# Kernel tuning notes

Measured on AMD Instinct MI355X. Metric: run time of the kernel, lower is better.

Reference implementation:

```python
import jax, jax.numpy as jnp
import numpy as np

N_NODES = 50000
N_EDGES = 800000
NODE_F = 100     # memory_feats
EDGE_F = 100     # raw edge feature dim
TIME_D = 100     # temporal encoder dimension
HEADS = 2
OUT_F = 100
NEG_SLOPE = 0.2


def setup_inputs() -> dict:
    key = jax.random.key(0)
    ks = jax.random.split(key, 16)
    return {
        'memory': jax.random.normal(ks[0], (N_NODES, NODE_F), jnp.float32),
        'node_ts': jax.random.uniform(ks[1], (N_NODES,), jnp.float32),
        'edge_feats_raw': jax.random.normal(ks[2], (N_EDGES, EDGE_F), jnp.float32),
        'edge_ts': jax.random.uniform(ks[3], (N_EDGES,), jnp.float32),
        'time_w': jax.random.normal(ks[4], (TIME_D,), jnp.float32),
        'time_b': jax.random.normal(ks[5], (TIME_D,), jnp.float32),
        'fc_node_w': jax.random.normal(ks[6], (NODE_F, HEADS * OUT_F), jnp.float32) * 0.1,
        'fc_node_b': jax.random.normal(ks[7], (HEADS * OUT_F,), jnp.float32) * 0.1,
        'fc_edge_w': jax.random.normal(ks[8], (EDGE_F + TIME_D, HEADS * OUT_F), jnp.float32) * 0.1,
        'fc_edge_b': jax.random.normal(ks[9], (HEADS * OUT_F,), jnp.float32) * 0.1,
        'attn_l': jax.random.normal(ks[10], (HEADS, OUT_F), jnp.float32) * 0.1,
        'attn_r': jax.random.normal(ks[11], (HEADS, OUT_F), jnp.float32) * 0.1,
        'attn_e': jax.random.normal(ks[12], (HEADS, OUT_F), jnp.float32) * 0.1,
        'src': jax.random.randint(ks[13], (N_EDGES,), 0, N_NODES, jnp.int32),
        'dst': jax.random.randint(ks[14], (N_EDGES,), 0, N_NODES, jnp.int32),
    }


def _forward(memory, node_ts, edge_feats_raw, edge_ts,
             time_w, time_b, fc_node_w, fc_node_b, fc_edge_w, fc_edge_b,
             attn_l, attn_r, attn_e, src, dst):
    n = memory.shape[0]
    # TemporalEdgePreprocess: Fourier time encoding of (edge_ts - ts[src])
    time_diff = edge_ts - node_ts[src]                                  # [E]
    te = jnp.cos(time_diff[:, None] * time_w[None, :] + time_b[None, :])  # [E, T]
    efeat = jnp.concatenate([edge_feats_raw, te], axis=1)               # [E, EDGE_F+T]

    # EdgeGATConv (eval mode: dropouts are identity)
    node_feat = (memory @ fc_node_w + fc_node_b).reshape(n, HEADS, OUT_F)          # [N,H,F]
    edge_feat = (efeat @ fc_edge_w + fc_edge_b).reshape(-1, HEADS, OUT_F)          # [E,H,F]

    el = jnp.einsum('nhf,hf->nh', node_feat, attn_l)   # [N,H]
    er = jnp.einsum('nhf,hf->nh', node_feat, attn_r)   # [N,H]
    ee = jnp.einsum('ehf,hf->eh', edge_feat, attn_e)   # [E,H]

    el_prime = el[src] + ee                             # u_add_e  [E,H]
    e = el_prime + er[dst]                              # e_add_v  [E,H]
    e = jnp.where(e > 0, e, NEG_SLOPE * e)              # leaky_relu

    # edge_softmax: softmax over incoming edges per destination node, per head
    emax = jax.ops.segment_max(e, dst, num_segments=n)  # [N,H]
    emax = jnp.where(jnp.isfinite(emax), emax, 0.0)     # zero-in-degree safety
    e_exp = jnp.exp(e - emax[dst])                      # [E,H]
    denom = jax.ops.segment_sum(e_exp, dst, num_segments=n)  # [N,H]
    a = e_exp / denom[dst]                              # [E,H]

    # msg_fn: m = a * el_prime (el_prime has singleton feature dim in torch code)
    m = a * el_prime                                    # [E,H]
    ft = jax.ops.segment_sum(m, dst, num_segments=n)    # [N,H]  (== [N,H,1] features)

    # residual: Identity since memory_feats == out_feats -> view(N,-1,F) = [N,1,F]
    rst = ft[:, :, None] + memory[:, None, :]           # [N,H,F] via broadcast
    return rst.mean(axis=1)                             # .mean(1) over heads -> [N,F]


def reference(memory, node_ts, edge_feats_raw, edge_ts,
              time_w, time_b, fc_node_w, fc_node_b, fc_edge_w, fc_edge_b,
              attn_l, attn_r, attn_e, src, dst):
    return _forward(memory, node_ts, edge_feats_raw, edge_ts,
                    time_w, time_b, fc_node_w, fc_node_b, fc_edge_w, fc_edge_b,
                    attn_l, attn_r, attn_e, src, dst)
```

## Files before the change

kernel.cpp:

```cpp
#include <hip/hip_runtime.h>


constexpr int F = 100;
constexpr float NEG_SLOPE = 0.2f;
constexpr int EPB = 32;

__device__ __forceinline__ float wave_reduce(float v) {
#pragma unroll
    for (int off = 32; off > 0; off >>= 1)
        v += __shfl_down(v, off, 64);
    return v;
}

__global__ void precompute_kernel(
    const float* __restrict__ fc_node_w, const float* __restrict__ fc_node_b,
    const float* __restrict__ fc_edge_w, const float* __restrict__ fc_edge_b,
    const float* __restrict__ attn_l, const float* __restrict__ attn_r,
    const float* __restrict__ attn_e,
    float4* __restrict__ w_node, float2* __restrict__ w_edge,
    float* __restrict__ bias)
{
    int wid  = blockIdx.x * (blockDim.x >> 6) + (threadIdx.x >> 6);
    int lane = threadIdx.x & 63;
    if (wid < F) {
        int t = wid;
        float a0 = 0.f, a1 = 0.f, a2 = 0.f, a3 = 0.f;
        for (int f = lane; f < F; f += 64) {
            float w0 = fc_node_w[t * 2 * F + f];
            float w1 = fc_node_w[t * 2 * F + F + f];
            a0 += w0 * attn_l[f];
            a1 += w1 * attn_l[F + f];
            a2 += w0 * attn_r[f];
            a3 += w1 * attn_r[F + f];
        }
        a0 = wave_reduce(a0); a1 = wave_reduce(a1);
        a2 = wave_reduce(a2); a3 = wave_reduce(a3);
        if (lane == 0) w_node[t] = make_float4(a0, a1, a2, a3);
    } else if (wid < 3 * F) {
        int t = wid - F;
        float a0 = 0.f, a1 = 0.f;
        for (int f = lane; f < F; f += 64) {
            a0 += fc_edge_w[t * 2 * F + f] * attn_e[f];
            a1 += fc_edge_w[t * 2 * F + F + f] * attn_e[F + f];
        }
        a0 = wave_reduce(a0); a1 = wave_reduce(a1);
        if (lane == 0) w_edge[t] = make_float2(a0, a1);
    } else if (wid < 3 * F + 6) {
        int j = wid - 3 * F;
        const float* b  = (j < 4) ? fc_node_b : fc_edge_b;
        const float* av = (j < 2) ? attn_l : (j < 4 ? attn_r : attn_e);
        int h = j & 1;
        float a0 = 0.f;
        for (int f = lane; f < F; f += 64)
            a0 += b[h * F + f] * av[h * F + f];
        a0 = wave_reduce(a0);
        if (lane == 0) bias[j] = a0;
    }
}

__global__ void node_kernel(const float* __restrict__ memory,
                            const float4* __restrict__ w_node,
                            const float* __restrict__ bias,
                            float4* __restrict__ el_er,
                            int* __restrict__ cnt, int N)
{
    int n    = blockIdx.x * (blockDim.x >> 6) + (threadIdx.x >> 6);
    int lane = threadIdx.x & 63;
    if (n >= N) return;
    const float* mrow = memory + (size_t)n * F;
    float a0 = 0.f, a1 = 0.f, a2 = 0.f, a3 = 0.f;
    for (int k = lane; k < F; k += 64) {
        float m  = mrow[k];
        float4 w = w_node[k];
        a0 += m * w.x; a1 += m * w.y; a2 += m * w.z; a3 += m * w.w;
    }
    a0 = wave_reduce(a0); a1 = wave_reduce(a1);
    a2 = wave_reduce(a2); a3 = wave_reduce(a3);
    if (lane == 0)
        el_er[n] = make_float4(a0 + bias[0], a1 + bias[1],
                               a2 + bias[2], a3 + bias[3]);
    if (lane == 1)
        cnt[n] = 0;
}

__global__ void count_kernel(const int* __restrict__ dst,
                             int* __restrict__ cnt, int E)
{
    int i = blockIdx.x * blockDim.x + threadIdx.x;
    if (i < E) atomicAdd(&cnt[dst[i]], 1);
}

__global__ void scan1_kernel(const int* __restrict__ cnt,
                             int* __restrict__ offs,
                             int* __restrict__ bsum, int N)
{
    __shared__ int tmp[256];
    int i = blockIdx.x * 256 + threadIdx.x;
    int v = (i < N) ? cnt[i] : 0;
    tmp[threadIdx.x] = v;
    __syncthreads();
    for (int d = 1; d < 256; d <<= 1) {
        int t = (threadIdx.x >= d) ? tmp[threadIdx.x - d] : 0;
        __syncthreads();
        tmp[threadIdx.x] += t;
        __syncthreads();
    }
    if (i < N) offs[i] = tmp[threadIdx.x] - v;
    if (threadIdx.x == 255) bsum[blockIdx.x] = tmp[255];
}

__global__ void scan2_kernel(int* __restrict__ bsum, int nb)
{
    __shared__ int tmp[256];
    int v = (threadIdx.x < nb) ? bsum[threadIdx.x] : 0;
    tmp[threadIdx.x] = v;
    __syncthreads();
    for (int d = 1; d < 256; d <<= 1) {
        int t = (threadIdx.x >= d) ? tmp[threadIdx.x - d] : 0;
        __syncthreads();
        tmp[threadIdx.x] += t;
        __syncthreads();
    }
    if (threadIdx.x < nb) bsum[threadIdx.x] = tmp[threadIdx.x] - v;
}

__global__ void scan3_kernel(int* __restrict__ offs,
                             const int* __restrict__ bsum,
                             int* __restrict__ cursor, int N)
{
    int i = blockIdx.x * 256 + threadIdx.x;
    if (i < N) {
        int o = offs[i] + bsum[blockIdx.x];
        offs[i]   = o;
        cursor[i] = o;
    }
}

__global__ void edge_gemv_kernel(
    const float* __restrict__ edge_raw,
    const float* __restrict__ edge_ts,
    const float* __restrict__ node_ts,
    const int* __restrict__ src,
    const int* __restrict__ dst,
    const float* __restrict__ time_w,
    const float* __restrict__ time_b,
    const float2* __restrict__ w_edge,
    const float* __restrict__ bias,
    const float4* __restrict__ el_er,
    int* __restrict__ cursor,
    float4* __restrict__ bucket, int E)
{
    __shared__ float4 wx4[25], wy4[25], wz4[25], ww4[25], tw4[25], tb4[25];
    __shared__ float  td_s[EPB];
    __shared__ float2 el_s[EPB];
    __shared__ float2 er_s[EPB];
    __shared__ int    d_s[EPB];

    const int  t  = threadIdx.x;
    const long eb = (long)blockIdx.x * EPB;

    if (t < 25) {
        float4 x, y, z, w, tw, tb;
#pragma unroll
        for (int j = 0; j < 4; ++j) {
            int k = 4 * t + j;
            float2 wr = w_edge[k];
            float2 wt = w_edge[F + k];
            ((float*)&x)[j]  = wr.x;  ((float*)&y)[j]  = wr.y;
            ((float*)&z)[j]  = wt.x;  ((float*)&w)[j]  = wt.y;
            ((float*)&tw)[j] = time_w[k];
            ((float*)&tb)[j] = time_b[k];
        }
        wx4[t] = x; wy4[t] = y; wz4[t] = z; ww4[t] = w;
        tw4[t] = tw; tb4[t] = tb;
    } else if (t >= 64 && t < 64 + EPB) {
        int  l = t - 64;
        long e = eb + l;
        if (e < E) {
            int s = src[e], d = dst[e];
            d_s[l]  = d;
            td_s[l] = edge_ts[e] - node_ts[s];
            float4 a = el_er[s];
            float4 b = el_er[d];
            el_s[l] = make_float2(a.x, a.y);
            er_s[l] = make_float2(b.z, b.w);
        }
    }
    __syncthreads();

    const int  el_ = t >> 3;
    const int  s8  = t & 7;
    const long e   = eb + el_;
    float a0 = 0.f, a1 = 0.f;
    if (e < E) {
        const float  td   = td_s[el_];
        const float4* row = (const float4*)edge_raw + e * 25;
#pragma unroll
        for (int i = 0; i < 4; ++i) {
            int c = s8 + 8 * i;
            if (c < 25) {
                float4 r  = row[c];
                float4 x  = wx4[c], y = wy4[c], z = wz4[c], w = ww4[c];
                float4 tw = tw4[c], tb = tb4[c];
                float c0 = __cosf(fmaf(td, tw.x, tb.x));
                float c1 = __cosf(fmaf(td, tw.y, tb.y));
                float c2 = __cosf(fmaf(td, tw.z, tb.z));
                float c3 = __cosf(fmaf(td, tw.w, tb.w));
                a0 = fmaf(r.x, x.x, fmaf(c0, z.x, a0));
                a1 = fmaf(r.x, y.x, fmaf(c0, w.x, a1));
                a0 = fmaf(r.y, x.y, fmaf(c1, z.y, a0));
                a1 = fmaf(r.y, y.y, fmaf(c1, w.y, a1));
                a0 = fmaf(r.z, x.z, fmaf(c2, z.z, a0));
                a1 = fmaf(r.z, y.z, fmaf(c2, w.z, a1));
                a0 = fmaf(r.w, x.w, fmaf(c3, z.w, a0));
                a1 = fmaf(r.w, y.w, fmaf(c3, w.w, a1));
            }
        }
    }
    a0 += __shfl_down(a0, 4, 64);  a1 += __shfl_down(a1, 4, 64);
    a0 += __shfl_down(a0, 2, 64);  a1 += __shfl_down(a1, 2, 64);
    a0 += __shfl_down(a0, 1, 64);  a1 += __shfl_down(a1, 1, 64);

    if (s8 == 0 && e < E) {
        float elp0 = el_s[el_].x + a0 + bias[4];
        float elp1 = el_s[el_].y + a1 + bias[5];
        float e0 = elp0 + er_s[el_].x;
        float e1 = elp1 + er_s[el_].y;
        e0 = e0 > 0.f ? e0 : NEG_SLOPE * e0;
        e1 = e1 > 0.f ? e1 : NEG_SLOPE * e1;
        float x0 = __expf(e0);
        float x1 = __expf(e1);
        int pos = atomicAdd(&cursor[d_s[el_]], 1);
        bucket[pos] = make_float4(x0 * elp0, x1 * elp1, x0, x1);
    }
}

__global__ void reduce_kernel(const float4* __restrict__ bucket,
                              const int* __restrict__ offs,
                              const int* __restrict__ cnt,
                              float* __restrict__ addbuf, int N)
{
    int g = blockIdx.x * (blockDim.x >> 4) + (threadIdx.x >> 4);
    int l = threadIdx.x & 15;
    if (g >= N) return;
    int base = offs[g];
    int deg  = cnt[g];
    float s0 = 0.f, s1 = 0.f, s2 = 0.f, s3 = 0.f;
    for (int j = l; j < deg; j += 16) {
        float4 v = bucket[base + j];
        s0 += v.x; s1 += v.y; s2 += v.z; s3 += v.w;
    }
    s0 += __shfl_down(s0, 8, 64); s1 += __shfl_down(s1, 8, 64);
    s2 += __shfl_down(s2, 8, 64); s3 += __shfl_down(s3, 8, 64);
    s0 += __shfl_down(s0, 4, 64); s1 += __shfl_down(s1, 4, 64);
    s2 += __shfl_down(s2, 4, 64); s3 += __shfl_down(s3, 4, 64);
    s0 += __shfl_down(s0, 2, 64); s1 += __shfl_down(s1, 2, 64);
    s2 += __shfl_down(s2, 2, 64); s3 += __shfl_down(s3, 2, 64);
    s0 += __shfl_down(s0, 1, 64); s1 += __shfl_down(s1, 1, 64);
    s2 += __shfl_down(s2, 1, 64); s3 += __shfl_down(s3, 1, 64);
    if (l == 0) {
        float ft0 = (s2 != 0.f) ? s0 / s2 : 0.f;
        float ft1 = (s3 != 0.f) ? s1 / s3 : 0.f;
        addbuf[g] = 0.5f * (ft0 + ft1);
    }
}

__global__ void out_kernel(const float* __restrict__ memory,
                           const float* __restrict__ addbuf,
                           float* __restrict__ out, int N)
{
    int i = blockIdx.x * blockDim.x + threadIdx.x;
    int total = N * (F / 2);
    if (i >= total) return;
    int n = i / (F / 2);
    float add = addbuf[n];
    float2 m = ((const float2*)memory)[i];
    float2 o;
    o.x = m.x + add;
    o.y = m.y + add;
    ((float2*)out)[i] = o;
}

extern "C" void kernel_launch(void* const* d_in, const int* in_sizes, int n_in,
                              void* d_out, int out_size, void* d_ws, size_t ws_size,
                              hipStream_t stream)
{
    const float* memory     = (const float*)d_in[0];
    const float* node_ts    = (const float*)d_in[1];
    const float* edge_raw   = (const float*)d_in[2];
    const float* edge_ts    = (const float*)d_in[3];
    const float* time_w     = (const float*)d_in[4];
    const float* time_b     = (const float*)d_in[5];
    const float* fc_node_w  = (const float*)d_in[6];
    const float* fc_node_b  = (const float*)d_in[7];
    const float* fc_edge_w  = (const float*)d_in[8];
    const float* fc_edge_b  = (const float*)d_in[9];
    const float* attn_l     = (const float*)d_in[10];
    const float* attn_r     = (const float*)d_in[11];
    const float* attn_e     = (const float*)d_in[12];
    const int*   src        = (const int*)d_in[13];
    const int*   dst        = (const int*)d_in[14];
    float*       out        = (float*)d_out;

    const int N = in_sizes[1];
    const int E = in_sizes[3];

    float* ws = (float*)d_ws;
    float4* w_node  = (float4*)ws;
    float2* w_edge  = (float2*)(ws + 400);
    float*  bias    = ws + 800;
    float4* el_er   = (float4*)(ws + 816);
    float*  addbuf  = ws + 816 + 4 * (size_t)N;
    int*    cnt     = (int*)(ws + 816 + 5 * (size_t)N);
    int*    offs    = cnt + N;
    int*    cursor  = offs + N;
    int*    bsum    = cursor + N;
    size_t  boff    = 816 + 8 * (size_t)N + 256;
    boff            = (boff + 3) & ~(size_t)3;
    float4* bucket  = (float4*)(ws + boff);

    const int nb = (N + 255) / 256;

    {
        int waves  = 3 * F + 6;
        int blocks = (waves + 3) / 4;
        precompute_kernel<<<blocks, 256, 0, stream>>>(
            fc_node_w, fc_node_b, fc_edge_w, fc_edge_b,
            attn_l, attn_r, attn_e, w_node, w_edge, bias);
    }
    {
        int blocks = (N + 3) / 4;
        node_kernel<<<blocks, 256, 0, stream>>>(
            memory, w_node, bias, el_er, cnt, N);
    }
    {
        int blocks = (E + 255) / 256;
        count_kernel<<<blocks, 256, 0, stream>>>(dst, cnt, E);
    }
    scan1_kernel<<<nb, 256, 0, stream>>>(cnt, offs, bsum, N);
    scan2_kernel<<<1, 256, 0, stream>>>(bsum, nb);
    scan3_kernel<<<nb, 256, 0, stream>>>(offs, bsum, cursor, N);
    {
        int blocks = (E + EPB - 1) / EPB;
        edge_gemv_kernel<<<blocks, 256, 0, stream>>>(
            edge_raw, edge_ts, node_ts, src, dst, time_w, time_b,
            w_edge, bias, el_er, cursor, bucket, E);
    }
    {
        int blocks = (N + 15) / 16;
        reduce_kernel<<<blocks, 256, 0, stream>>>(bucket, offs, cnt, addbuf, N);
    }
    {
        int total  = N * (F / 2);
        int blocks = (total + 255) / 256;
        out_kernel<<<blocks, 256, 0, stream>>>(memory, addbuf, out, N);
    }
}
```

Before: 553.1 us.

## Fuse small kernels to cut launch count and intermediate traffic

```diff
diff --git a/kernel.cpp b/kernel.cpp
--- a/kernel.cpp
+++ b/kernel.cpp
@@ -18,7 +18,8 @@
     const float* __restrict__ attn_l, const float* __restrict__ attn_r,
     const float* __restrict__ attn_e,
     float4* __restrict__ w_node, float2* __restrict__ w_edge,
-    float* __restrict__ bias)
+    float* __restrict__ bias,
+    int* __restrict__ cnt, int N)
 {
     int wid  = blockIdx.x * (blockDim.x >> 6) + (threadIdx.x >> 6);
     int lane = threadIdx.x & 63;
@@ -56,38 +57,39 @@
         a0 = wave_reduce(a0);
         if (lane == 0) bias[j] = a0;
     }
-}
-
-__global__ void node_kernel(const float* __restrict__ memory,
-                            const float4* __restrict__ w_node,
-                            const float* __restrict__ bias,
-                            float4* __restrict__ el_er,
-                            int* __restrict__ cnt, int N)
-{
-    int n    = blockIdx.x * (blockDim.x >> 6) + (threadIdx.x >> 6);
-    int lane = threadIdx.x & 63;
-    if (n >= N) return;
-    const float* mrow = memory + (size_t)n * F;
-    float a0 = 0.f, a1 = 0.f, a2 = 0.f, a3 = 0.f;
-    for (int k = lane; k < F; k += 64) {
-        float m  = mrow[k];
-        float4 w = w_node[k];
-        a0 += m * w.x; a1 += m * w.y; a2 += m * w.z; a3 += m * w.w;
-    }
-    a0 = wave_reduce(a0); a1 = wave_reduce(a1);
-    a2 = wave_reduce(a2); a3 = wave_reduce(a3);
-    if (lane == 0)
-        el_er[n] = make_float4(a0 + bias[0], a1 + bias[1],
-                               a2 + bias[2], a3 + bias[3]);
-    if (lane == 1)
-        cnt[n] = 0;
-}
-
-__global__ void count_kernel(const int* __restrict__ dst,
-                             int* __restrict__ cnt, int E)
-{
-    int i = blockIdx.x * blockDim.x + threadIdx.x;
-    if (i < E) atomicAdd(&cnt[dst[i]], 1);
+    for (int i = blockIdx.x * blockDim.x + threadIdx.x; i < N;
+         i += gridDim.x * blockDim.x)
+        cnt[i] = 0;
+}
+
+__global__ void node_count_kernel(const float* __restrict__ memory,
+                                  const float4* __restrict__ w_node,
+                                  const float* __restrict__ bias,
+                                  float4* __restrict__ el_er,
+                                  const int* __restrict__ dst,
+                                  int* __restrict__ cnt,
+                                  int N, int E, int nodeBlocks)
+{
+    if ((int)blockIdx.x < nodeBlocks) {
+        int n    = blockIdx.x * (blockDim.x >> 6) + (threadIdx.x >> 6);
+        int lane = threadIdx.x & 63;
+        if (n >= N) return;
+        const float* mrow = memory + (size_t)n * F;
+        float a0 = 0.f, a1 = 0.f, a2 = 0.f, a3 = 0.f;
+        for (int k = lane; k < F; k += 64) {
+            float m  = mrow[k];
+            float4 w = w_node[k];
+            a0 += m * w.x; a1 += m * w.y; a2 += m * w.z; a3 += m * w.w;
+        }
+        a0 = wave_reduce(a0); a1 = wave_reduce(a1);
+        a2 = wave_reduce(a2); a3 = wave_reduce(a3);
+        if (lane == 0)
+            el_er[n] = make_float4(a0 + bias[0], a1 + bias[1],
+                                   a2 + bias[2], a3 + bias[3]);
+    } else {
+        int i = (blockIdx.x - nodeBlocks) * blockDim.x + threadIdx.x;
+        if (i < E) atomicAdd(&cnt[dst[i]], 1);
+    }
 }
 
 __global__ void scan1_kernel(const int* __restrict__ cnt,
@@ -109,28 +111,25 @@
     if (threadIdx.x == 255) bsum[blockIdx.x] = tmp[255];
 }
 
-__global__ void scan2_kernel(int* __restrict__ bsum, int nb)
+__global__ void scan23_kernel(int* __restrict__ offs,
+                              const int* __restrict__ bsum,
+                              int* __restrict__ cursor, int N, int nb)
 {
     __shared__ int tmp[256];
-    int v = (threadIdx.x < nb) ? bsum[threadIdx.x] : 0;
-    tmp[threadIdx.x] = v;
+    int t = threadIdx.x;
+    int v = (t < nb) ? bsum[t] : 0;
+    tmp[t] = v;
     __syncthreads();
     for (int d = 1; d < 256; d <<= 1) {
-        int t = (threadIdx.x >= d) ? tmp[threadIdx.x - d] : 0;
+        int x = (t >= d) ? tmp[t - d] : 0;
         __syncthreads();
-        tmp[threadIdx.x] += t;
+        tmp[t] += x;
         __syncthreads();
     }
-    if (threadIdx.x < nb) bsum[threadIdx.x] = tmp[threadIdx.x] - v;
-}
-
-__global__ void scan3_kernel(int* __restrict__ offs,
-                             const int* __restrict__ bsum,
-                             int* __restrict__ cursor, int N)
-{
-    int i = blockIdx.x * 256 + threadIdx.x;
+    int boff = (blockIdx.x == 0) ? 0 : tmp[blockIdx.x - 1];
+    int i = blockIdx.x * 256 + t;
     if (i < N) {
-        int o = offs[i] + bsum[blockIdx.x];
+        int o = offs[i] + boff;
         offs[i]   = o;
         cursor[i] = o;
     }
@@ -235,10 +234,11 @@
     }
 }
 
-__global__ void reduce_kernel(const float4* __restrict__ bucket,
-                              const int* __restrict__ offs,
-                              const int* __restrict__ cnt,
-                              float* __restrict__ addbuf, int N)
+__global__ void reduce_out_kernel(const float4* __restrict__ bucket,
+                                  const int* __restrict__ offs,
+                                  const int* __restrict__ cnt,
+                                  const float* __restrict__ memory,
+                                  float* __restrict__ out, int N)
 {
     int g = blockIdx.x * (blockDim.x >> 4) + (threadIdx.x >> 4);
     int l = threadIdx.x & 15;
@@ -258,27 +258,21 @@
     s2 += __shfl_down(s2, 2, 64); s3 += __shfl_down(s3, 2, 64);
     s0 += __shfl_down(s0, 1, 64); s1 += __shfl_down(s1, 1, 64);
     s2 += __shfl_down(s2, 1, 64); s3 += __shfl_down(s3, 1, 64);
-    if (l == 0) {
-        float ft0 = (s2 != 0.f) ? s0 / s2 : 0.f;
-        float ft1 = (s3 != 0.f) ? s1 / s3 : 0.f;
-        addbuf[g] = 0.5f * (ft0 + ft1);
-    }
-}
-
-__global__ void out_kernel(const float* __restrict__ memory,
-                           const float* __restrict__ addbuf,
-                           float* __restrict__ out, int N)
-{
-    int i = blockIdx.x * blockDim.x + threadIdx.x;
-    int total = N * (F / 2);
-    if (i >= total) return;
-    int n = i / (F / 2);
-    float add = addbuf[n];
-    float2 m = ((const float2*)memory)[i];
-    float2 o;
-    o.x = m.x + add;
-    o.y = m.y + add;
-    ((float2*)out)[i] = o;
+    float ft0 = (s2 != 0.f) ? s0 / s2 : 0.f;
+    float ft1 = (s3 != 0.f) ? s1 / s3 : 0.f;
+    float add = 0.5f * (ft0 + ft1);
+    add = __shfl(add, 0, 16);
+
+    const float4* m4 = (const float4*)(memory + (size_t)g * F);
+    float4*       o4 = (float4*)(out + (size_t)g * F);
+#pragma unroll
+    for (int c = l; c < F / 4; c += 16) {
+        float4 m = m4[c];
+        float4 o;
+        o.x = m.x + add; o.y = m.y + add;
+        o.z = m.z + add; o.w = m.w + add;
+        o4[c] = o;
+    }
 }
 
 extern "C" void kernel_launch(void* const* d_in, const int* in_sizes, int n_in,
@@ -310,7 +304,6 @@
     float2* w_edge  = (float2*)(ws + 400);
     float*  bias    = ws + 800;
     float4* el_er   = (float4*)(ws + 816);
-    float*  addbuf  = ws + 816 + 4 * (size_t)N;
     int*    cnt     = (int*)(ws + 816 + 5 * (size_t)N);
     int*    offs    = cnt + N;
     int*    cursor  = offs + N;
@@ -322,24 +315,20 @@
     const int nb = (N + 255) / 256;
 
     {
-        int waves  = 3 * F + 6;
-        int blocks = (waves + 3) / 4;
+        int wblocks = (3 * F + 6 + 3) / 4;
+        int blocks  = (nb > wblocks) ? nb : wblocks;
         precompute_kernel<<<blocks, 256, 0, stream>>>(
             fc_node_w, fc_node_b, fc_edge_w, fc_edge_b,
-            attn_l, attn_r, attn_e, w_node, w_edge, bias);
+            attn_l, attn_r, attn_e, w_node, w_edge, bias, cnt, N);
     }
     {
-        int blocks = (N + 3) / 4;
-        node_kernel<<<blocks, 256, 0, stream>>>(
-            memory, w_node, bias, el_er, cnt, N);
-    }
-    {
-        int blocks = (E + 255) / 256;
-        count_kernel<<<blocks, 256, 0, stream>>>(dst, cnt, E);
+        int nodeBlocks  = (N + 3) / 4;
+        int countBlocks = (E + 255) / 256;
+        node_count_kernel<<<nodeBlocks + countBlocks, 256, 0, stream>>>(
+            memory, w_node, bias, el_er, dst, cnt, N, E, nodeBlocks);
     }
     scan1_kernel<<<nb, 256, 0, stream>>>(cnt, offs, bsum, N);
-    scan2_kernel<<<1, 256, 0, stream>>>(bsum, nb);
-    scan3_kernel<<<nb, 256, 0, stream>>>(offs, bsum, cursor, N);
+    scan23_kernel<<<nb, 256, 0, stream>>>(offs, bsum, cursor, N, nb);
     {
         int blocks = (E + EPB - 1) / EPB;
         edge_gemv_kernel<<<blocks, 256, 0, stream>>>(
@@ -348,11 +337,7 @@
     }
     {
         int blocks = (N + 15) / 16;
-        reduce_kernel<<<blocks, 256, 0, stream>>>(bucket, offs, cnt, addbuf, N);
-    }
-    {
-        int total  = N * (F / 2);
-        int blocks = (total + 255) / 256;
-        out_kernel<<<blocks, 256, 0, stream>>>(memory, addbuf, out, N);
-    }
-}
+        reduce_out_kernel<<<blocks, 256, 0, stream>>>(
+            bucket, offs, cnt, memory, out, N);
+    }
+}
```

Result: no change. 547.3 us, median of 2 (-1.0%).
